# Performance work log

Measured on AMD Instinct MI355X. Metric: run time of the kernel, lower is better.

The kernel has to match this reference:

```python
import jax, jax.numpy as jnp
import numpy as np
import math

N_NODES = 100000
N_EDGES = 1600000
IN_C, HID_C, OUT_C = 512, 128, 64
N_LAYERS = 8
ALPHA = 0.1
THETA = 0.5


def setup_inputs() -> dict:
    key = jax.random.key(0)
    ks = jax.random.split(key, 6)
    x = jax.random.normal(ks[0], (N_NODES, IN_C), dtype=jnp.float32)
    edge_index = jax.random.randint(ks[1], (2, N_EDGES), 0, N_NODES, dtype=jnp.int32)
    edge_weight = jax.random.uniform(ks[2], (N_EDGES,), dtype=jnp.float32)
    # parameters (scaled for numerical sanity)
    W_enc = jax.random.normal(ks[3], (HID_C, IN_C), dtype=jnp.float32) * (1.0 / math.sqrt(IN_C))
    W_convs = jax.random.normal(ks[4], (N_LAYERS, HID_C, HID_C), dtype=jnp.float32) * (1.0 / math.sqrt(HID_C))
    W_dec = jax.random.normal(ks[5], (OUT_C, HID_C), dtype=jnp.float32) * (1.0 / math.sqrt(HID_C))
    return {"x": x, "edge_index": edge_index, "edge_weight": edge_weight,
            "W_enc": W_enc, "W_convs": W_convs, "W_dec": W_dec}


def reference(x, edge_index, edge_weight, W_enc, W_convs, W_dec):
    # eval mode: dropout is a no-op
    src, dst = edge_index[0], edge_index[1]
    h = x @ W_enc.T                      # [N, HID]
    x0 = h                               # initial residual
    for i in range(N_LAYERS):
        # sparse neighbor aggregation: agg[d] = sum_e w_e * h[src_e]
        msg = h[src] * edge_weight[:, None]                      # [E, HID]
        agg = jax.ops.segment_sum(msg, dst, num_segments=N_NODES)
        hh = (1.0 - ALPHA) * agg + ALPHA * x0                    # initial residual
        beta = math.log(THETA / (i + 1) + 1.0)                   # identity mapping weight
        h = jax.nn.relu((1.0 - beta) * hh + beta * (hh @ W_convs[i]))
    return h @ W_dec.T                   # [N, OUT]
```

## Files before the change

### kernel.cpp

```cpp
#include <hip/hip_runtime.h>
#include <math.h>

#define N_NODES 100000
#define N_EDGES 1600000
#define IN_C 512
#define HID_C 128
#define OUT_C 64
#define N_LAYERS 8

typedef short bf16x8 __attribute__((ext_vector_type(8)));
typedef float f32x4 __attribute__((ext_vector_type(4)));

static __device__ __forceinline__ ushort f2bf(float f) {
  uint u = __float_as_uint(f);
  u = (u + 0x7FFFu + ((u >> 16) & 1u)) >> 16;
  return (ushort)u;
}
static __device__ __forceinline__ float bflo(uint u) { return __uint_as_float(u << 16); }
static __device__ __forceinline__ float bfhi(uint u) { return __uint_as_float(u & 0xffff0000u); }

__global__ __launch_bounds__(256) void hist_kernel(const int* __restrict__ dst,
                                                   int* __restrict__ cnt) {
  int e = blockIdx.x * 256 + threadIdx.x;
  atomicAdd(&cnt[dst[e]], 1);
}

__global__ __launch_bounds__(256) void scan_block(const int* __restrict__ in,
                                                  int* __restrict__ out,
                                                  int* __restrict__ bsum, int n) {
  __shared__ int tsum[256];
  int t = threadIdx.x;
  int base = blockIdx.x * 1024 + t * 4;
  int v0 = (base + 0 < n) ? in[base + 0] : 0;
  int v1 = (base + 1 < n) ? in[base + 1] : 0;
  int v2 = (base + 2 < n) ? in[base + 2] : 0;
  int v3 = (base + 3 < n) ? in[base + 3] : 0;
  int s = v0 + v1 + v2 + v3;
  tsum[t] = s;
  __syncthreads();
  for (int off = 1; off < 256; off <<= 1) {
    int x = (t >= off) ? tsum[t - off] : 0;
    __syncthreads();
    tsum[t] += x;
    __syncthreads();
  }
  int excl = tsum[t] - s;
  int i0 = excl + v0, i1 = i0 + v1, i2 = i1 + v2, i3 = i2 + v3;
  if (base + 0 < n) out[base + 0] = i0;
  if (base + 1 < n) out[base + 1] = i1;
  if (base + 2 < n) out[base + 2] = i2;
  if (base + 3 < n) out[base + 3] = i3;
  if (t == 255 && bsum) bsum[blockIdx.x] = tsum[255];
}

__global__ __launch_bounds__(256) void finalize_rows(const int* __restrict__ incl,
                                                     const int* __restrict__ auxi,
                                                     int* __restrict__ row, int n) {
  int i = blockIdx.x * 256 + threadIdx.x;
  if (i < n) {
    int g = i >> 10;
    int off = g ? auxi[g - 1] : 0;
    row[i + 1] = incl[i] + off;
    if (i == 0) row[0] = 0;
  }
}

__global__ __launch_bounds__(256) void init_cursor(const int* __restrict__ row,
                                                   int* __restrict__ cur, int n) {
  int i = blockIdx.x * 256 + threadIdx.x;
  if (i < n) cur[i] = row[i];
}

__global__ __launch_bounds__(256) void fill_csr(const int* __restrict__ src,
                                                const int* __restrict__ dst,
                                                const float* __restrict__ w,
                                                int* __restrict__ cur,
                                                uint* __restrict__ epk) {
  int e = blockIdx.x * 256 + threadIdx.x;
  int d = dst[e];
  int p = atomicAdd(&cur[d], 1);
  uint fb = __float_as_uint(w[e]) + 0x8000u;
  epk[p] = ((fb >> 16) << 17) | (uint)src[e];
}

__global__ __launch_bounds__(256) void cast_weights(const float* __restrict__ we,
                                                    const float* __restrict__ wc,
                                                    const float* __restrict__ wd,
                                                    ushort* __restrict__ web,
                                                    ushort* __restrict__ wcb,
                                                    ushort* __restrict__ wdb) {
  int i = blockIdx.x * 256 + threadIdx.x;
  if (i < 128 * 512) web[i] = f2bf(we[i]);
  if (i < 8 * 128 * 128) {
    int layer = i >> 14, rem = i & 16383, k = rem >> 7, j = rem & 127;
    wcb[(layer << 14) + (j << 7) + k] = f2bf(wc[i]);
  }
  if (i < 64 * 128) wdb[i] = f2bf(wd[i]);
}

__global__ __launch_bounds__(256) void enc_mfma(const float* __restrict__ x,
                                                const ushort* __restrict__ wb,
                                                ushort* __restrict__ h) {
  __shared__ ushort xs[32][136];
  __shared__ ushort ws[128][136];
  int tid = threadIdx.x;
  size_t row0 = (size_t)blockIdx.x * 32;
  int lane = tid & 63;
  int wv = tid >> 6;
  int m0 = (wv >> 1) * 16;
  int n0 = (wv & 1) * 64;
  int arow = m0 + (lane & 15);
  int akb = (lane >> 4) * 8;
  f32x4 acc[4] = {};
  for (int kc = 0; kc < 4; kc++) {
    int k0 = kc * 128;
    __syncthreads();
#pragma unroll
    for (int i = 0; i < 4; i++) {
      int u = tid + i * 256;
      int r = u >> 5, c4 = u & 31;
      float4 v = *(const float4*)(x + (row0 + r) * IN_C + k0 + c4 * 4);
      uint2 p;
      p.x = (uint)f2bf(v.x) | ((uint)f2bf(v.y) << 16);
      p.y = (uint)f2bf(v.z) | ((uint)f2bf(v.w) << 16);
      *(uint2*)&xs[r][c4 * 4] = p;
    }
#pragma unroll
    for (int i = 0; i < 8; i++) {
      int u = tid + i * 256;
      int c = u >> 4, o = u & 15;
      *(uint4*)&ws[c][o * 8] = *(const uint4*)(wb + (size_t)c * IN_C + k0 + o * 8);
    }
    __syncthreads();
#pragma unroll
    for (int ks = 0; ks < 4; ks++) {
      int kk = ks * 32 + akb;
      bf16x8 a = *(bf16x8*)&xs[arow][kk];
#pragma unroll
      for (int n = 0; n < 4; n++) {
        bf16x8 b = *(bf16x8*)&ws[n0 + n * 16 + (lane & 15)][kk];
        acc[n] = __builtin_amdgcn_mfma_f32_16x16x32_bf16(a, b, acc[n], 0, 0, 0);
      }
    }
  }
  int crow = m0 + (lane >> 4) * 4;
  int ccol = lane & 15;
#pragma unroll
  for (int n = 0; n < 4; n++)
#pragma unroll
    for (int r = 0; r < 4; r++)
      h[(row0 + crow + r) * HID_C + n0 + n * 16 + ccol] = f2bf(acc[n][r]);
}

__global__ __launch_bounds__(256) void agg_bf(const ushort* __restrict__ h,
                                              const ushort* __restrict__ x0,
                                              const int* __restrict__ row,
                                              const uint* __restrict__ epk,
                                              ushort* __restrict__ out) {
  int node = (blockIdx.x * 256 + threadIdx.x) >> 6;
  int lane = threadIdx.x & 63;
  int beg = row[node], end = row[node + 1];
  float a0 = 0.f, a1 = 0.f;
  const uint* hp = (const uint*)h + lane;
  int e = beg;
  for (; e + 4 <= end; e += 4) {
    uint p0 = epk[e + 0];
    uint p1 = epk[e + 1];
    uint p2 = epk[e + 2];
    uint p3 = epk[e + 3];
    uint h0 = hp[(size_t)(p0 & 0x1FFFFu) * 64];
    uint h1 = hp[(size_t)(p1 & 0x1FFFFu) * 64];
    uint h2 = hp[(size_t)(p2 & 0x1FFFFu) * 64];
    uint h3 = hp[(size_t)(p3 & 0x1FFFFu) * 64];
    float w0 = __uint_as_float((p0 >> 17) << 16);
    float w1 = __uint_as_float((p1 >> 17) << 16);
    float w2 = __uint_as_float((p2 >> 17) << 16);
    float w3 = __uint_as_float((p3 >> 17) << 16);
    a0 = fmaf(w0, bflo(h0), a0); a1 = fmaf(w0, bfhi(h0), a1);
    a0 = fmaf(w1, bflo(h1), a0); a1 = fmaf(w1, bfhi(h1), a1);
    a0 = fmaf(w2, bflo(h2), a0); a1 = fmaf(w2, bfhi(h2), a1);
    a0 = fmaf(w3, bflo(h3), a0); a1 = fmaf(w3, bfhi(h3), a1);
  }
  for (; e < end; e++) {
    uint p = epk[e];
    uint hv = hp[(size_t)(p & 0x1FFFFu) * 64];
    float w = __uint_as_float((p >> 17) << 16);
    a0 = fmaf(w, bflo(hv), a0);
    a1 = fmaf(w, bfhi(hv), a1);
  }
  uint xv = ((const uint*)x0)[(size_t)node * 64 + lane];
  float o0 = 0.9f * a0 + 0.1f * bflo(xv);
  float o1 = 0.9f * a1 + 0.1f * bfhi(xv);
  ((uint*)out)[(size_t)node * 64 + lane] = (uint)f2bf(o0) | ((uint)f2bf(o1) << 16);
}

__global__ __launch_bounds__(256) void conv_mfma(ushort* __restrict__ hbuf,
                                                 const ushort* __restrict__ wb,
                                                 float onemb, float beta) {
  __shared__ ushort hs[32][136];
  __shared__ ushort ws[128][136];
  int tid = threadIdx.x;
  size_t row0 = (size_t)blockIdx.x * 32;
  {
    int r = tid >> 3, o = tid & 7;
    *(uint4*)&hs[r][o * 16] = *(const uint4*)(hbuf + (row0 + r) * HID_C + o * 16);
    *(uint4*)&hs[r][o * 16 + 8] = *(const uint4*)(hbuf + (row0 + r) * HID_C + o * 16 + 8);
  }
#pragma unroll
  for (int i = 0; i < 8; i++) {
    int u = tid + i * 256;
    int c = u >> 4, o = u & 15;
    *(uint4*)&ws[c][o * 8] = *(const uint4*)(wb + (size_t)c * HID_C + o * 8);
  }
  __syncthreads();
  int lane = tid & 63;
  int wv = tid >> 6;
  int m0 = (wv >> 1) * 16, n0 = (wv & 1) * 64;
  int arow = m0 + (lane & 15), akb = (lane >> 4) * 8;
  f32x4 acc[4] = {};
#pragma unroll
  for (int ks = 0; ks < 4; ks++) {
    int kk = ks * 32 + akb;
    bf16x8 a = *(bf16x8*)&hs[arow][kk];
#pragma unroll
    for (int n = 0; n < 4; n++) {
      bf16x8 b = *(bf16x8*)&ws[n0 + n * 16 + (lane & 15)][kk];
      acc[n] = __builtin_amdgcn_mfma_f32_16x16x32_bf16(a, b, acc[n], 0, 0, 0);
    }
  }
  __syncthreads();
  int crow = m0 + (lane >> 4) * 4, ccol = lane & 15;
#pragma unroll
  for (int n = 0; n < 4; n++)
#pragma unroll
    for (int r = 0; r < 4; r++) {
      float hv = bflo((uint)hs[crow + r][n0 + n * 16 + ccol]);
      float o = fmaxf(onemb * hv + beta * acc[n][r], 0.f);
      hbuf[(row0 + crow + r) * HID_C + n0 + n * 16 + ccol] = f2bf(o);
    }
}

__global__ __launch_bounds__(256) void dec_mfma(const ushort* __restrict__ h,
                                                const ushort* __restrict__ wb,
                                                float* __restrict__ out) {
  __shared__ ushort hs[32][136];
  __shared__ ushort ws[64][136];
  int tid = threadIdx.x;
  size_t row0 = (size_t)blockIdx.x * 32;
  {
    int r = tid >> 3, o = tid & 7;
    *(uint4*)&hs[r][o * 16] = *(const uint4*)(h + (row0 + r) * HID_C + o * 16);
    *(uint4*)&hs[r][o * 16 + 8] = *(const uint4*)(h + (row0 + r) * HID_C + o * 16 + 8);
  }
#pragma unroll
  for (int i = 0; i < 4; i++) {
    int u = tid + i * 256;
    int c = u >> 4, o = u & 15;
    *(uint4*)&ws[c][o * 8] = *(const uint4*)(wb + (size_t)c * HID_C + o * 8);
  }
  __syncthreads();
  int lane = tid & 63, wv = tid >> 6;
  int m0 = (wv >> 1) * 16, n0 = (wv & 1) * 32;
  int arow = m0 + (lane & 15), akb = (lane >> 4) * 8;
  f32x4 acc[2] = {};
#pragma unroll
  for (int ks = 0; ks < 4; ks++) {
    int kk = ks * 32 + akb;
    bf16x8 a = *(bf16x8*)&hs[arow][kk];
#pragma unroll
    for (int n = 0; n < 2; n++) {
      bf16x8 b = *(bf16x8*)&ws[n0 + n * 16 + (lane & 15)][kk];
      acc[n] = __builtin_amdgcn_mfma_f32_16x16x32_bf16(a, b, acc[n], 0, 0, 0);
    }
  }
  int crow = m0 + (lane >> 4) * 4, ccol = lane & 15;
#pragma unroll
  for (int n = 0; n < 2; n++)
#pragma unroll
    for (int r = 0; r < 4; r++)
      out[(row0 + crow + r) * OUT_C + n0 + n * 16 + ccol] = acc[n][r];
}

extern "C" void kernel_launch(void* const* d_in, const int* in_sizes, int n_in,
                              void* d_out, int out_size, void* d_ws, size_t ws_size,
                              hipStream_t stream) {
  const float* x = (const float*)d_in[0];
  const int* ei = (const int*)d_in[1];
  const float* ew = (const float*)d_in[2];
  const float* Wenc = (const float*)d_in[3];
  const float* Wconvs = (const float*)d_in[4];
  const float* Wdec = (const float*)d_in[5];
  float* out = (float*)d_out;

  char* p = (char*)d_ws;
  ushort* H0 = (ushort*)p; p += (size_t)N_NODES * HID_C * 2;
  ushort* HA = (ushort*)p; p += (size_t)N_NODES * HID_C * 2;
  ushort* HB = (ushort*)p; p += (size_t)N_NODES * HID_C * 2;
  uint* EPK = (uint*)p;    p += (size_t)N_EDGES * 4;
  ushort* WENC = (ushort*)p;  p += 128 * 512 * 2;
  ushort* WCONV = (ushort*)p; p += 8 * 128 * 128 * 2;
  ushort* WDEC = (ushort*)p;  p += 64 * 128 * 2;
  int* ROW = (int*)p;  p += (N_NODES + 1) * 4;
  int* CNT = (int*)p;  p += N_NODES * 4;
  int* INCL = (int*)p; p += N_NODES * 4;
  int* CUR = (int*)p;  p += N_NODES * 4;
  int* AUX = (int*)p;  p += 128 * 4;
  int* AUXI = (int*)p;

  const int* src = ei;
  const int* dst = ei + N_EDGES;

  cast_weights<<<512, 256, 0, stream>>>(Wenc, Wconvs, Wdec, WENC, WCONV, WDEC);

  hipMemsetAsync(CNT, 0, N_NODES * sizeof(int), stream);
  hist_kernel<<<N_EDGES / 256, 256, 0, stream>>>(dst, CNT);
  scan_block<<<98, 256, 0, stream>>>(CNT, INCL, AUX, N_NODES);
  scan_block<<<1, 256, 0, stream>>>(AUX, AUXI, nullptr, 98);
  finalize_rows<<<391, 256, 0, stream>>>(INCL, AUXI, ROW, N_NODES);
  init_cursor<<<391, 256, 0, stream>>>(ROW, CUR, N_NODES);
  fill_csr<<<N_EDGES / 256, 256, 0, stream>>>(src, dst, ew, CUR, EPK);

  enc_mfma<<<3125, 256, 0, stream>>>(x, WENC, H0);

  const ushort* cur = H0;
  ushort* bufs[2] = {HA, HB};
  for (int i = 0; i < N_LAYERS; i++) {
    ushort* nxt = bufs[i & 1];
    agg_bf<<<25000, 256, 0, stream>>>(cur, H0, ROW, EPK, nxt);
    float beta = logf(0.5f / (float)(i + 1) + 1.0f);
    conv_mfma<<<3125, 256, 0, stream>>>(nxt, WCONV + (size_t)i * HID_C * HID_C,
                                        1.0f - beta, beta);
    cur = nxt;
  }

  dec_mfma<<<3125, 256, 0, stream>>>(cur, WDEC, out);
}
```

Measured before the change: 922.7 us.

## Fuse neighbor aggregation into conv MFMA kernel via shared-memory tile

```diff
diff --git a/kernel.cpp b/kernel.cpp
--- a/kernel.cpp
+++ b/kernel.cpp
@@ -152,69 +152,73 @@
       h[(row0 + crow + r) * HID_C + n0 + n * 16 + ccol] = f2bf(acc[n][r]);
 }
 
-__global__ __launch_bounds__(256) void agg_bf(const ushort* __restrict__ h,
-                                              const ushort* __restrict__ x0,
-                                              const int* __restrict__ row,
-                                              const uint* __restrict__ epk,
-                                              ushort* __restrict__ out) {
-  int node = (blockIdx.x * 256 + threadIdx.x) >> 6;
-  int lane = threadIdx.x & 63;
-  int beg = row[node], end = row[node + 1];
-  float a0 = 0.f, a1 = 0.f;
-  const uint* hp = (const uint*)h + lane;
-  int e = beg;
-  for (; e + 4 <= end; e += 4) {
-    uint p0 = epk[e + 0];
-    uint p1 = epk[e + 1];
-    uint p2 = epk[e + 2];
-    uint p3 = epk[e + 3];
-    uint h0 = hp[(size_t)(p0 & 0x1FFFFu) * 64];
-    uint h1 = hp[(size_t)(p1 & 0x1FFFFu) * 64];
-    uint h2 = hp[(size_t)(p2 & 0x1FFFFu) * 64];
-    uint h3 = hp[(size_t)(p3 & 0x1FFFFu) * 64];
-    float w0 = __uint_as_float((p0 >> 17) << 16);
-    float w1 = __uint_as_float((p1 >> 17) << 16);
-    float w2 = __uint_as_float((p2 >> 17) << 16);
-    float w3 = __uint_as_float((p3 >> 17) << 16);
-    a0 = fmaf(w0, bflo(h0), a0); a1 = fmaf(w0, bfhi(h0), a1);
-    a0 = fmaf(w1, bflo(h1), a0); a1 = fmaf(w1, bfhi(h1), a1);
-    a0 = fmaf(w2, bflo(h2), a0); a1 = fmaf(w2, bfhi(h2), a1);
-    a0 = fmaf(w3, bflo(h3), a0); a1 = fmaf(w3, bfhi(h3), a1);
-  }
-  for (; e < end; e++) {
-    uint p = epk[e];
-    uint hv = hp[(size_t)(p & 0x1FFFFu) * 64];
-    float w = __uint_as_float((p >> 17) << 16);
-    a0 = fmaf(w, bflo(hv), a0);
-    a1 = fmaf(w, bfhi(hv), a1);
-  }
-  uint xv = ((const uint*)x0)[(size_t)node * 64 + lane];
-  float o0 = 0.9f * a0 + 0.1f * bflo(xv);
-  float o1 = 0.9f * a1 + 0.1f * bfhi(xv);
-  ((uint*)out)[(size_t)node * 64 + lane] = (uint)f2bf(o0) | ((uint)f2bf(o1) << 16);
-}
-
-__global__ __launch_bounds__(256) void conv_mfma(ushort* __restrict__ hbuf,
-                                                 const ushort* __restrict__ wb,
-                                                 float onemb, float beta) {
+__global__ __launch_bounds__(256) void agg_conv(const ushort* __restrict__ h,
+                                                const ushort* __restrict__ x0,
+                                                const int* __restrict__ row,
+                                                const uint* __restrict__ epk,
+                                                const ushort* __restrict__ wb,
+                                                ushort* __restrict__ out,
+                                                float onemb, float beta) {
   __shared__ ushort hs[32][136];
   __shared__ ushort ws[128][136];
   int tid = threadIdx.x;
-  size_t row0 = (size_t)blockIdx.x * 32;
-  {
-    int r = tid >> 3, o = tid & 7;
-    *(uint4*)&hs[r][o * 16] = *(const uint4*)(hbuf + (row0 + r) * HID_C + o * 16);
-    *(uint4*)&hs[r][o * 16 + 8] = *(const uint4*)(hbuf + (row0 + r) * HID_C + o * 16 + 8);
-  }
+  int lane = tid & 63;
+  int wv = tid >> 6;
+  int node0 = blockIdx.x * 32;
+
 #pragma unroll
   for (int i = 0; i < 8; i++) {
     int u = tid + i * 256;
     int c = u >> 4, o = u & 15;
     *(uint4*)&ws[c][o * 8] = *(const uint4*)(wb + (size_t)c * HID_C + o * 8);
   }
+
+  const uint* hp = (const uint*)h + lane;
+  for (int i = 0; i < 8; i++) {
+    int node = node0 + wv * 8 + i;
+    int beg = row[node], end = row[node + 1];
+    float a0 = 0.f, a1 = 0.f;
+    for (int e = beg; e < end; e += 8) {
+      uint p0 = (e + 0 < end) ? epk[e + 0] : 0u;
+      uint p1 = (e + 1 < end) ? epk[e + 1] : 0u;
+      uint p2 = (e + 2 < end) ? epk[e + 2] : 0u;
+      uint p3 = (e + 3 < end) ? epk[e + 3] : 0u;
+      uint p4 = (e + 4 < end) ? epk[e + 4] : 0u;
+      uint p5 = (e + 5 < end) ? epk[e + 5] : 0u;
+      uint p6 = (e + 6 < end) ? epk[e + 6] : 0u;
+      uint p7 = (e + 7 < end) ? epk[e + 7] : 0u;
+      uint h0 = hp[(size_t)(p0 & 0x1FFFFu) * 64];
+      uint h1 = hp[(size_t)(p1 & 0x1FFFFu) * 64];
+      uint h2 = hp[(size_t)(p2 & 0x1FFFFu) * 64];
+      uint h3 = hp[(size_t)(p3 & 0x1FFFFu) * 64];
+      uint h4 = hp[(size_t)(p4 & 0x1FFFFu) * 64];
+      uint h5 = hp[(size_t)(p5 & 0x1FFFFu) * 64];
+      uint h6 = hp[(size_t)(p6 & 0x1FFFFu) * 64];
+      uint h7 = hp[(size_t)(p7 & 0x1FFFFu) * 64];
+      float w0 = __uint_as_float((p0 >> 17) << 16);
+      float w1 = __uint_as_float((p1 >> 17) << 16);
+      float w2 = __uint_as_float((p2 >> 17) << 16);
+      float w3 = __uint_as_float((p3 >> 17) << 16);
+      float w4 = __uint_as_float((p4 >> 17) << 16);
+      float w5 = __uint_as_float((p5 >> 17) << 16);
+      float w6 = __uint_as_float((p6 >> 17) << 16);
+      float w7 = __uint_as_float((p7 >> 17) << 16);
+      a0 = fmaf(w0, bflo(h0), a0); a1 = fmaf(w0, bfhi(h0), a1);
+      a0 = fmaf(w1, bflo(h1), a0); a1 = fmaf(w1, bfhi(h1), a1);
+      a0 = fmaf(w2, bflo(h2), a0); a1 = fmaf(w2, bfhi(h2), a1);
+      a0 = fmaf(w3, bflo(h3), a0); a1 = fmaf(w3, bfhi(h3), a1);
+      a0 = fmaf(w4, bflo(h4), a0); a1 = fmaf(w4, bfhi(h4), a1);
+      a0 = fmaf(w5, bflo(h5), a0); a1 = fmaf(w5, bfhi(h5), a1);
+      a0 = fmaf(w6, bflo(h6), a0); a1 = fmaf(w6, bfhi(h6), a1);
+      a0 = fmaf(w7, bflo(h7), a0); a1 = fmaf(w7, bfhi(h7), a1);
+    }
+    uint xv = ((const uint*)x0)[(size_t)node * 64 + lane];
+    float o0 = 0.9f * a0 + 0.1f * bflo(xv);
+    float o1 = 0.9f * a1 + 0.1f * bfhi(xv);
+    ((uint*)&hs[wv * 8 + i][0])[lane] = (uint)f2bf(o0) | ((uint)f2bf(o1) << 16);
+  }
   __syncthreads();
-  int lane = tid & 63;
-  int wv = tid >> 6;
+
   int m0 = (wv >> 1) * 16, n0 = (wv & 1) * 64;
   int arow = m0 + (lane & 15), akb = (lane >> 4) * 8;
   f32x4 acc[4] = {};
@@ -228,7 +232,6 @@
       acc[n] = __builtin_amdgcn_mfma_f32_16x16x32_bf16(a, b, acc[n], 0, 0, 0);
     }
   }
-  __syncthreads();
   int crow = m0 + (lane >> 4) * 4, ccol = lane & 15;
 #pragma unroll
   for (int n = 0; n < 4; n++)
@@ -236,7 +239,7 @@
     for (int r = 0; r < 4; r++) {
       float hv = bflo((uint)hs[crow + r][n0 + n * 16 + ccol]);
       float o = fmaxf(onemb * hv + beta * acc[n][r], 0.f);
-      hbuf[(row0 + crow + r) * HID_C + n0 + n * 16 + ccol] = f2bf(o);
+      out[(size_t)(node0 + crow + r) * HID_C + n0 + n * 16 + ccol] = f2bf(o);
     }
 }
 
@@ -326,10 +329,10 @@
   ushort* bufs[2] = {HA, HB};
   for (int i = 0; i < N_LAYERS; i++) {
     ushort* nxt = bufs[i & 1];
-    agg_bf<<<25000, 256, 0, stream>>>(cur, H0, ROW, EPK, nxt);
     float beta = logf(0.5f / (float)(i + 1) + 1.0f);
-    conv_mfma<<<3125, 256, 0, stream>>>(nxt, WCONV + (size_t)i * HID_C * HID_C,
-                                        1.0f - beta, beta);
+    agg_conv<<<3125, 256, 0, stream>>>(cur, H0, ROW, EPK,
+                                       WCONV + (size_t)i * HID_C * HID_C, nxt,
+                                       1.0f - beta, beta);
     cur = nxt;
   }
 
```

After: 1.153 ms. 1.25x slower.
